# Kernel optimization log

Measured on AMD Instinct MI355X. Metric: run time of the kernel, lower is better.

Reference implementation:

```python
import jax, jax.numpy as jnp
import numpy as np

COMMITMENT_COST = 0.25
NUM_EMBEDDINGS = 8192
EMBEDDING_DIM = 256


def setup_inputs() -> dict:
    key = jax.random.key(0)
    k1, k2 = jax.random.split(key)
    inputs = jax.random.normal(k1, (32, 256, EMBEDDING_DIM), dtype=jnp.float32)
    codebook = jax.random.normal(k2, (NUM_EMBEDDINGS, EMBEDDING_DIM), dtype=jnp.float32)
    # match nn.Embedding init: N(0,1) then L2-normalize rows
    codebook = codebook / jnp.linalg.norm(codebook, axis=1, keepdims=True)
    return {"inputs": inputs, "codebook": codebook}


def reference(inputs, codebook):
    B, K, D = inputs.shape
    flat = inputs.reshape(-1, D).astype(jnp.float32)  # [N, D], N = B*K
    N = flat.shape[0]

    distances = (
        jnp.sum(flat * flat, axis=1, keepdims=True)
        + jnp.sum(codebook * codebook, axis=1)
        - 2.0 * flat @ codebook.T
    )
    indices = jnp.argmin(distances, axis=1)  # [N]

    # codebook lookup (equivalent to one-hot @ codebook)
    quantized = codebook[indices].reshape(B, K, D)

    e_latent_loss = jnp.mean((jax.lax.stop_gradient(quantized) - inputs) ** 2)
    q_latent_loss = jnp.mean((quantized - jax.lax.stop_gradient(inputs)) ** 2)
    loss = q_latent_loss + COMMITMENT_COST * e_latent_loss

    # straight-through estimator
    quantized_ste = inputs + jax.lax.stop_gradient(quantized - inputs)

    # perplexity from codebook usage histogram (== mean of one-hot encodings)
    counts = jnp.zeros((NUM_EMBEDDINGS,), dtype=jnp.float32).at[indices].add(1.0)
    avg_probs = counts / N
    perplexity = jnp.exp(-jnp.sum(avg_probs * jnp.log(avg_probs + 1e-10)))

    return quantized_ste, loss, perplexity
```

## Files before the change

kernel.cpp:

```cpp
#include <hip/hip_runtime.h>
#include <math.h>

#define NTOK 8192
#define NEMB 8192
#define DIM  256

typedef _Float16 f16x8 __attribute__((ext_vector_type(8)));
typedef _Float16 f16x4 __attribute__((ext_vector_type(4)));
typedef float    f32x4 __attribute__((ext_vector_type(4)));

__global__ __launch_bounds__(256) void convert_kernel(
        const float* __restrict__ X, const float* __restrict__ C,
        _Float16* __restrict__ Xh, _Float16* __restrict__ Ch,
        float* __restrict__ cnorm, float* __restrict__ xnorm,
        unsigned long long* __restrict__ keys, int* __restrict__ counts) {
    const bool isC = (blockIdx.y != 0);
    if (isC && blockIdx.x < 8) {
        ((int4*)counts)[blockIdx.x * 256 + threadIdx.x] = make_int4(0, 0, 0, 0);
    }
    if (!isC && blockIdx.x < 8) {
        int4 ff = make_int4(-1, -1, -1, -1);
        ((int4*)keys)[blockIdx.x * 512 + threadIdx.x * 2]     = ff;
        ((int4*)keys)[blockIdx.x * 512 + threadIdx.x * 2 + 1] = ff;
    }
    const float* src = isC ? C : X;
    _Float16* dst = isC ? Ch : Xh;
    size_t t = (size_t)blockIdx.x * 256 + threadIdx.x;
    float4 x = *(const float4*)&src[t * 4];
    f16x4 h;
    h[0] = (_Float16)x.x; h[1] = (_Float16)x.y;
    h[2] = (_Float16)x.z; h[3] = (_Float16)x.w;
    *(f16x4*)&dst[t * 4] = h;
    float s = x.x * x.x + x.y * x.y + x.z * x.z + x.w * x.w;
    #pragma unroll
    for (int off = 32; off >= 1; off >>= 1) s += __shfl_xor(s, off);
    if ((threadIdx.x & 63) == 0) {
        if (isC) cnorm[t >> 6] = s; else xnorm[t >> 6] = s;
    }
}

__device__ __forceinline__ int swz(int row) { return (row + (row >> 2)) & 3; }

__device__ __forceinline__ void stage_pair32(
        const _Float16* __restrict__ Ag, const _Float16* __restrict__ Bg,
        _Float16* pair, int t) {
    #pragma unroll
    for (int c = 0; c < 2; ++c) {
        int gr  = c * 256 + t;
        int row = gr >> 2;
        int kg  = (gr & 3) ^ swz(row);
        __builtin_amdgcn_global_load_lds(
            (const __attribute__((address_space(1))) void*)(Ag + (size_t)row * DIM + kg * 8),
            (__attribute__((address_space(3))) void*)(pair + (size_t)gr * 8), 16, 0, 0);
        __builtin_amdgcn_global_load_lds(
            (const __attribute__((address_space(1))) void*)(Bg + (size_t)row * DIM + kg * 8),
            (__attribute__((address_space(3))) void*)(pair + 4096 + (size_t)gr * 8), 16, 0, 0);
    }
}

__device__ __forceinline__ void compute_pair32(
        const _Float16* pair, f32x4 (&acc)[4][4],
        int wm, int wn, int lrow, int g) {
    const _Float16* Abase = pair;
    const _Float16* Bbase = pair + 4096;
    f16x8 af[4], bf_[4];
    #pragma unroll
    for (int tm = 0; tm < 4; ++tm) {
        int row = wm + tm * 16 + lrow;
        af[tm] = *(const f16x8*)&Abase[(row * 4 + (g ^ swz(row))) * 8];
    }
    #pragma unroll
    for (int tn = 0; tn < 4; ++tn) {
        int row = wn + tn * 16 + lrow;
        bf_[tn] = *(const f16x8*)&Bbase[(row * 4 + (g ^ swz(row))) * 8];
    }
    #pragma unroll
    for (int tm = 0; tm < 4; ++tm)
        #pragma unroll
        for (int tn = 0; tn < 4; ++tn)
            acc[tm][tn] = __builtin_amdgcn_mfma_f32_16x16x32_f16(
                af[tm], bf_[tn], acc[tm][tn], 0, 0, 0);
}

__global__ __launch_bounds__(256) void mfma_argmin_kernel(
        const _Float16* __restrict__ Xh, const _Float16* __restrict__ Ch,
        const float* __restrict__ cnorm,
        unsigned long long* __restrict__ keys) {
    __shared__ __align__(16) _Float16 lds[16384];

    const int t = threadIdx.x;
    const int wid = t >> 6, lane = t & 63;
    const int tb0 = blockIdx.x * 128;
    const int cb0 = blockIdx.y * 128;
    const int wm = (wid >> 1) * 64;
    const int wn = (wid & 1) * 64;
    const int lrow = lane & 15;
    const int g = lane >> 4;

    float cn[16];
    #pragma unroll
    for (int tm = 0; tm < 4; ++tm)
        #pragma unroll
        for (int reg = 0; reg < 4; ++reg)
            cn[tm * 4 + reg] = cnorm[cb0 + wm + tm * 16 + g * 4 + reg];

    f32x4 acc[4][4];
    #pragma unroll
    for (int a = 0; a < 4; ++a)
        #pragma unroll
        for (int b = 0; b < 4; ++b) acc[a][b] = (f32x4)0.0f;

    const _Float16* Ag = Ch + (size_t)cb0 * DIM;
    const _Float16* Bg = Xh + (size_t)tb0 * DIM;

    stage_pair32(Ag, Bg, lds, t);
    __syncthreads();
    #pragma unroll
    for (int p = 0; p < 8; ++p) {
        _Float16* cur = lds + (p & 1) * 8192;
        if (p < 7) {
            _Float16* nxt = lds + ((p + 1) & 1) * 8192;
            stage_pair32(Ag + (p + 1) * 32, Bg + (p + 1) * 32, nxt, t);
        }
        compute_pair32(cur, acc, wm, wn, lrow, g);
        __syncthreads();
    }

    float* cmb_v = (float*)lds;
    int*   cmb_i = (int*)((float*)lds + 256);

    #pragma unroll
    for (int tn = 0; tn < 4; ++tn) {
        float bv = 1e30f; int bi = 0x7fffffff;
        #pragma unroll
        for (int tm = 0; tm < 4; ++tm) {
            #pragma unroll
            for (int reg = 0; reg < 4; ++reg) {
                float d = fmaf(-2.0f, acc[tm][tn][reg], cn[tm * 4 + reg]);
                int code = cb0 + wm + tm * 16 + g * 4 + reg;
                if (d < bv) { bv = d; bi = code; }
            }
        }
        #pragma unroll
        for (int off = 16; off <= 32; off <<= 1) {
            float ov = __shfl_xor(bv, off);
            int   oi = __shfl_xor(bi, off);
            if (ov < bv || (ov == bv && oi < bi)) { bv = ov; bi = oi; }
        }
        if (g == 0) {
            int tl = wn + tn * 16 + lrow;
            cmb_v[tl * 2 + (wid >> 1)] = bv;
            cmb_i[tl * 2 + (wid >> 1)] = bi;
        }
    }
    __syncthreads();
    if (t < 128) {
        float v0 = cmb_v[t * 2], v1 = cmb_v[t * 2 + 1];
        int   i0 = cmb_i[t * 2], i1 = cmb_i[t * 2 + 1];
        bool tk = (v1 < v0) || (v1 == v0 && i1 < i0);
        float bv = tk ? v1 : v0;
        int   bi = tk ? i1 : i0;
        unsigned long long key =
            ((unsigned long long)__builtin_bit_cast(unsigned, bv + 64.0f) << 32)
            | (unsigned)bi;
        atomicMin(&keys[tb0 + t], key);
    }
}

__global__ __launch_bounds__(256) void gather_kernel(
        const float* __restrict__ C, const unsigned long long* __restrict__ keys,
        const float* __restrict__ xnorm, int* __restrict__ counts,
        float* __restrict__ out, float* __restrict__ psum) {
    __shared__ int idx_lds[32];
    const int m0 = blockIdx.x * 32;
    const int t = threadIdx.x;
    if (t < 32) {
        unsigned long long k = keys[m0 + t];
        int bi  = (int)(unsigned)k;
        float d = __builtin_bit_cast(float, (unsigned)(k >> 32)) - 64.0f;
        idx_lds[t] = bi;
        atomicAdd(&counts[bi], 1);
        float lt = d + xnorm[m0 + t];
        #pragma unroll
        for (int off = 1; off < 32; off <<= 1) lt += __shfl_xor(lt, off);
        if (t == 0) psum[blockIdx.x] = lt;
    }
    __syncthreads();
    const int wid = t >> 6, lane = t & 63;
    #pragma unroll
    for (int r = 0; r < 8; ++r) {
        int token = m0 + wid * 8 + r;
        int e = idx_lds[wid * 8 + r];
        float4 q = *(const float4*)&C[(size_t)e * DIM + lane * 4];
        *(float4*)&out[(size_t)token * DIM + lane * 4] = q;
    }
}

__global__ __launch_bounds__(256) void finalize_kernel(
        const int* __restrict__ counts, const float* __restrict__ psum,
        float* __restrict__ out) {
    const int t = threadIdx.x;
    double local = 0.0;
    #pragma unroll 1
    for (int e = t; e < NEMB; e += 256) {
        float p = (float)counts[e] * (1.0f / (float)NTOK);
        local += (double)(p * logf(p + 1e-10f));
    }
    float ls = psum[t];
    #pragma unroll
    for (int off = 32; off >= 1; off >>= 1) {
        local += __shfl_xor(local, off);
        ls    += __shfl_xor(ls, off);
    }
    __shared__ double she[4];
    __shared__ float  shs[4];
    int lane = t & 63, wid = t >> 6;
    if (lane == 0) { she[wid] = local; shs[wid] = ls; }
    __syncthreads();
    if (t == 0) {
        double ent = she[0] + she[1] + she[2] + she[3];
        float  ssq = shs[0] + shs[1] + shs[2] + shs[3];
        out[(size_t)NTOK * DIM]     = 1.25f * ssq / (float)((size_t)NTOK * DIM);
        out[(size_t)NTOK * DIM + 1] = expf((float)(-ent));
    }
}

extern "C" void kernel_launch(void* const* d_in, const int* in_sizes, int n_in,
                              void* d_out, int out_size, void* d_ws, size_t ws_size,
                              hipStream_t stream) {
    const float* X = (const float*)d_in[0];
    const float* C = (const float*)d_in[1];
    float* out = (float*)d_out;

    char* ws = (char*)d_ws;
    size_t o = 0;
    _Float16* Xh = (_Float16*)(ws + o); o += (size_t)NTOK * DIM * 2;
    _Float16* Ch = (_Float16*)(ws + o); o += (size_t)NEMB * DIM * 2;
    float* cnorm = (float*)(ws + o); o += (size_t)NEMB * 4;
    float* xnorm = (float*)(ws + o); o += (size_t)NTOK * 4;
    unsigned long long* keys = (unsigned long long*)(ws + o); o += (size_t)NTOK * 8;
    int* counts  = (int*)(ws + o);   o += (size_t)NEMB * 4;
    float* psum  = (float*)(ws + o);

    convert_kernel<<<dim3(NTOK * DIM / 4 / 256, 2), 256, 0, stream>>>(
        X, C, Xh, Ch, cnorm, xnorm, keys, counts);
    mfma_argmin_kernel<<<dim3(NTOK / 128, NEMB / 128), 256, 0, stream>>>(
        Xh, Ch, cnorm, keys);
    gather_kernel<<<256, 256, 0, stream>>>(
        C, keys, xnorm, counts, out, psum);
    finalize_kernel<<<1, 256, 0, stream>>>(counts, psum, out);
}
```

Baseline: 132.0 us.

## Fuse argmin and gather into one persistent kernel with a grid barrier

Each block now loops over four codebook tiles and keeps a running argmin in registers, so the grid shrinks to 1024 blocks and there are fewer global atomicMin operations. A software grid-wide barrier (an atomic counter spun on by thread 0) then lets the same kernel do the gather, histogram and loss accumulation. This removes the separate gather launch and the psum reduction path. The barrier assumes all 1024 blocks are co-resident, which launch_bounds(256,4) is meant to ensure; if they are not, the kernel deadlocks. Loss accumulation also moves to a single float atomicAdd.

```diff
diff --git a/kernel.cpp b/kernel.cpp
--- a/kernel.cpp
+++ b/kernel.cpp
@@ -4,6 +4,7 @@
 #define NTOK 8192
 #define NEMB 8192
 #define DIM  256
+#define GBLK 1024
 
 typedef _Float16 f16x8 __attribute__((ext_vector_type(8)));
 typedef _Float16 f16x4 __attribute__((ext_vector_type(4)));
@@ -17,6 +18,9 @@
     const bool isC = (blockIdx.y != 0);
     if (isC && blockIdx.x < 8) {
         ((int4*)counts)[blockIdx.x * 256 + threadIdx.x] = make_int4(0, 0, 0, 0);
+    }
+    if (isC && blockIdx.x == 8 && threadIdx.x < 2) {
+        counts[NEMB + threadIdx.x] = 0;
     }
     if (!isC && blockIdx.x < 8) {
         int4 ff = make_int4(-1, -1, -1, -1);
@@ -82,123 +86,139 @@
                 af[tm], bf_[tn], acc[tm][tn], 0, 0, 0);
 }
 
-__global__ __launch_bounds__(256) void mfma_argmin_kernel(
+__global__ __launch_bounds__(256, 4) void mfma_gather_kernel(
         const _Float16* __restrict__ Xh, const _Float16* __restrict__ Ch,
-        const float* __restrict__ cnorm,
-        unsigned long long* __restrict__ keys) {
+        const float* __restrict__ cnorm, const float* __restrict__ xnorm,
+        const float* __restrict__ C,
+        unsigned long long* __restrict__ keys, int* __restrict__ counts,
+        float* __restrict__ out) {
     __shared__ __align__(16) _Float16 lds[16384];
+
+    int* bar      = counts + NEMB;
+    float* lossac = (float*)(counts + NEMB + 1);
 
     const int t = threadIdx.x;
     const int wid = t >> 6, lane = t & 63;
     const int tb0 = blockIdx.x * 128;
-    const int cb0 = blockIdx.y * 128;
     const int wm = (wid >> 1) * 64;
     const int wn = (wid & 1) * 64;
     const int lrow = lane & 15;
     const int g = lane >> 4;
-
-    float cn[16];
-    #pragma unroll
-    for (int tm = 0; tm < 4; ++tm)
-        #pragma unroll
-        for (int reg = 0; reg < 4; ++reg)
-            cn[tm * 4 + reg] = cnorm[cb0 + wm + tm * 16 + g * 4 + reg];
-
-    f32x4 acc[4][4];
-    #pragma unroll
-    for (int a = 0; a < 4; ++a)
-        #pragma unroll
-        for (int b = 0; b < 4; ++b) acc[a][b] = (f32x4)0.0f;
-
-    const _Float16* Ag = Ch + (size_t)cb0 * DIM;
     const _Float16* Bg = Xh + (size_t)tb0 * DIM;
 
-    stage_pair32(Ag, Bg, lds, t);
-    __syncthreads();
-    #pragma unroll
-    for (int p = 0; p < 8; ++p) {
-        _Float16* cur = lds + (p & 1) * 8192;
-        if (p < 7) {
-            _Float16* nxt = lds + ((p + 1) & 1) * 8192;
-            stage_pair32(Ag + (p + 1) * 32, Bg + (p + 1) * 32, nxt, t);
+    float rbv = 1e30f; int rbi = 0x7fffffff;
+
+    #pragma unroll 1
+    for (int p4 = 0; p4 < 4; ++p4) {
+        const int cb0 = (blockIdx.y * 4 + p4) * 128;
+        const _Float16* Ag = Ch + (size_t)cb0 * DIM;
+
+        float cn[16];
+        #pragma unroll
+        for (int tm = 0; tm < 4; ++tm)
+            #pragma unroll
+            for (int reg = 0; reg < 4; ++reg)
+                cn[tm * 4 + reg] = cnorm[cb0 + wm + tm * 16 + g * 4 + reg];
+
+        f32x4 acc[4][4];
+        #pragma unroll
+        for (int a = 0; a < 4; ++a)
+            #pragma unroll
+            for (int b = 0; b < 4; ++b) acc[a][b] = (f32x4)0.0f;
+
+        stage_pair32(Ag, Bg, lds, t);
+        __syncthreads();
+        #pragma unroll
+        for (int p = 0; p < 8; ++p) {
+            _Float16* cur = lds + (p & 1) * 8192;
+            if (p < 7) {
+                stage_pair32(Ag + (p + 1) * 32, Bg + (p + 1) * 32,
+                             lds + ((p + 1) & 1) * 8192, t);
+            }
+            compute_pair32(cur, acc, wm, wn, lrow, g);
+            __syncthreads();
         }
-        compute_pair32(cur, acc, wm, wn, lrow, g);
+
+        float* cmb_v = (float*)lds;
+        int*   cmb_i = (int*)((float*)lds + 256);
+        #pragma unroll
+        for (int tn = 0; tn < 4; ++tn) {
+            float bv = 1e30f; int bi = 0x7fffffff;
+            #pragma unroll
+            for (int tm = 0; tm < 4; ++tm) {
+                #pragma unroll
+                for (int reg = 0; reg < 4; ++reg) {
+                    float d = fmaf(-2.0f, acc[tm][tn][reg], cn[tm * 4 + reg]);
+                    int code = cb0 + wm + tm * 16 + g * 4 + reg;
+                    if (d < bv) { bv = d; bi = code; }
+                }
+            }
+            #pragma unroll
+            for (int off = 16; off <= 32; off <<= 1) {
+                float ov = __shfl_xor(bv, off);
+                int   oi = __shfl_xor(bi, off);
+                if (ov < bv || (ov == bv && oi < bi)) { bv = ov; bi = oi; }
+            }
+            if (g == 0) {
+                int tl = wn + tn * 16 + lrow;
+                cmb_v[tl * 2 + (wid >> 1)] = bv;
+                cmb_i[tl * 2 + (wid >> 1)] = bi;
+            }
+        }
         __syncthreads();
-    }
-
-    float* cmb_v = (float*)lds;
-    int*   cmb_i = (int*)((float*)lds + 256);
-
-    #pragma unroll
-    for (int tn = 0; tn < 4; ++tn) {
-        float bv = 1e30f; int bi = 0x7fffffff;
-        #pragma unroll
-        for (int tm = 0; tm < 4; ++tm) {
-            #pragma unroll
-            for (int reg = 0; reg < 4; ++reg) {
-                float d = fmaf(-2.0f, acc[tm][tn][reg], cn[tm * 4 + reg]);
-                int code = cb0 + wm + tm * 16 + g * 4 + reg;
-                if (d < bv) { bv = d; bi = code; }
-            }
+        if (t < 128) {
+            float v0 = cmb_v[t * 2], v1 = cmb_v[t * 2 + 1];
+            int   i0 = cmb_i[t * 2], i1 = cmb_i[t * 2 + 1];
+            bool tk = (v1 < v0) || (v1 == v0 && i1 < i0);
+            float bv = tk ? v1 : v0;
+            int   bi = tk ? i1 : i0;
+            if (bv < rbv || (bv == rbv && bi < rbi)) { rbv = bv; rbi = bi; }
         }
-        #pragma unroll
-        for (int off = 16; off <= 32; off <<= 1) {
-            float ov = __shfl_xor(bv, off);
-            int   oi = __shfl_xor(bi, off);
-            if (ov < bv || (ov == bv && oi < bi)) { bv = ov; bi = oi; }
-        }
-        if (g == 0) {
-            int tl = wn + tn * 16 + lrow;
-            cmb_v[tl * 2 + (wid >> 1)] = bv;
-            cmb_i[tl * 2 + (wid >> 1)] = bi;
-        }
-    }
-    __syncthreads();
+        __syncthreads();
+    }
+
     if (t < 128) {
-        float v0 = cmb_v[t * 2], v1 = cmb_v[t * 2 + 1];
-        int   i0 = cmb_i[t * 2], i1 = cmb_i[t * 2 + 1];
-        bool tk = (v1 < v0) || (v1 == v0 && i1 < i0);
-        float bv = tk ? v1 : v0;
-        int   bi = tk ? i1 : i0;
         unsigned long long key =
-            ((unsigned long long)__builtin_bit_cast(unsigned, bv + 64.0f) << 32)
-            | (unsigned)bi;
+            ((unsigned long long)__builtin_bit_cast(unsigned, rbv + 64.0f) << 32)
+            | (unsigned)rbi;
         atomicMin(&keys[tb0 + t], key);
     }
-}
-
-__global__ __launch_bounds__(256) void gather_kernel(
-        const float* __restrict__ C, const unsigned long long* __restrict__ keys,
-        const float* __restrict__ xnorm, int* __restrict__ counts,
-        float* __restrict__ out, float* __restrict__ psum) {
-    __shared__ int idx_lds[32];
-    const int m0 = blockIdx.x * 32;
-    const int t = threadIdx.x;
-    if (t < 32) {
-        unsigned long long k = keys[m0 + t];
+    __syncthreads();
+
+    if (t == 0) {
+        __hip_atomic_fetch_add(bar, 1, __ATOMIC_ACQ_REL, __HIP_MEMORY_SCOPE_AGENT);
+        while (__hip_atomic_load(bar, __ATOMIC_ACQUIRE, __HIP_MEMORY_SCOPE_AGENT)
+               < GBLK) { }
+    }
+    __syncthreads();
+
+    int* idx_lds = (int*)lds;
+    const int bid = blockIdx.y * 64 + blockIdx.x;
+    const int m0 = bid * 8;
+    if (t < 8) {
+        unsigned long long k = atomicMin(&keys[m0 + t], ~0ull);
         int bi  = (int)(unsigned)k;
         float d = __builtin_bit_cast(float, (unsigned)(k >> 32)) - 64.0f;
         idx_lds[t] = bi;
         atomicAdd(&counts[bi], 1);
         float lt = d + xnorm[m0 + t];
-        #pragma unroll
-        for (int off = 1; off < 32; off <<= 1) lt += __shfl_xor(lt, off);
-        if (t == 0) psum[blockIdx.x] = lt;
-    }
-    __syncthreads();
-    const int wid = t >> 6, lane = t & 63;
-    #pragma unroll
-    for (int r = 0; r < 8; ++r) {
-        int token = m0 + wid * 8 + r;
-        int e = idx_lds[wid * 8 + r];
+        lt += __shfl_xor(lt, 1);
+        lt += __shfl_xor(lt, 2);
+        lt += __shfl_xor(lt, 4);
+        if (t == 0) atomicAdd(lossac, lt);
+    }
+    __syncthreads();
+    #pragma unroll
+    for (int r = 0; r < 2; ++r) {
+        int token = m0 + wid * 2 + r;
+        int e = idx_lds[wid * 2 + r];
         float4 q = *(const float4*)&C[(size_t)e * DIM + lane * 4];
         *(float4*)&out[(size_t)token * DIM + lane * 4] = q;
     }
 }
 
 __global__ __launch_bounds__(256) void finalize_kernel(
-        const int* __restrict__ counts, const float* __restrict__ psum,
-        float* __restrict__ out) {
+        const int* __restrict__ counts, float* __restrict__ out) {
     const int t = threadIdx.x;
     double local = 0.0;
     #pragma unroll 1
@@ -206,20 +226,15 @@
         float p = (float)counts[e] * (1.0f / (float)NTOK);
         local += (double)(p * logf(p + 1e-10f));
     }
-    float ls = psum[t];
-    #pragma unroll
-    for (int off = 32; off >= 1; off >>= 1) {
-        local += __shfl_xor(local, off);
-        ls    += __shfl_xor(ls, off);
-    }
+    #pragma unroll
+    for (int off = 32; off >= 1; off >>= 1) local += __shfl_xor(local, off);
     __shared__ double she[4];
-    __shared__ float  shs[4];
     int lane = t & 63, wid = t >> 6;
-    if (lane == 0) { she[wid] = local; shs[wid] = ls; }
+    if (lane == 0) she[wid] = local;
     __syncthreads();
     if (t == 0) {
         double ent = she[0] + she[1] + she[2] + she[3];
-        float  ssq = shs[0] + shs[1] + shs[2] + shs[3];
+        float ssq = ((const float*)(counts + NEMB + 1))[0];
         out[(size_t)NTOK * DIM]     = 1.25f * ssq / (float)((size_t)NTOK * DIM);
         out[(size_t)NTOK * DIM + 1] = expf((float)(-ent));
     }
@@ -239,14 +254,11 @@
     float* cnorm = (float*)(ws + o); o += (size_t)NEMB * 4;
     float* xnorm = (float*)(ws + o); o += (size_t)NTOK * 4;
     unsigned long long* keys = (unsigned long long*)(ws + o); o += (size_t)NTOK * 8;
-    int* counts  = (int*)(ws + o);   o += (size_t)NEMB * 4;
-    float* psum  = (float*)(ws + o);
+    int* counts  = (int*)(ws + o);   o += (size_t)(NEMB + 2) * 4;
 
     convert_kernel<<<dim3(NTOK * DIM / 4 / 256, 2), 256, 0, stream>>>(
         X, C, Xh, Ch, cnorm, xnorm, keys, counts);
-    mfma_argmin_kernel<<<dim3(NTOK / 128, NEMB / 128), 256, 0, stream>>>(
-        Xh, Ch, cnorm, keys);
-    gather_kernel<<<256, 256, 0, stream>>>(
-        C, keys, xnorm, counts, out, psum);
-    finalize_kernel<<<1, 256, 0, stream>>>(counts, psum, out);
-}
+    mfma_gather_kernel<<<dim3(64, 16), 256, 0, stream>>>(
+        Xh, Ch, cnorm, xnorm, C, keys, counts, out);
+    finalize_kernel<<<1, 256, 0, stream>>>(counts, out);
+}
```

Result: slower. 383.1 us (+190.2%).
